# Optimization experiments

Hardware: AMD Instinct MI355X
Metric: run time of the kernel (lower is better)

The kernel has to match this reference:

```python
import jax, jax.numpy as jnp
import numpy as np

N_NODES = 100000
N_EDGES = 1600000
F_IN, F_HID, F_OUT = 128, 128, 16
NEG_SLOPE = 0.2


def _glorot(key, shape):
    fan = sum(shape)
    return jax.random.uniform(key, shape, jnp.float32, -1.0, 1.0) * jnp.sqrt(6.0 / fan)


def setup_inputs() -> dict:
    key = jax.random.key(0)
    ks = jax.random.split(key, 16)
    x = jax.random.normal(ks[0], (N_NODES, F_IN), jnp.float32)
    edge_index = jax.random.randint(ks[1], (2, N_EDGES), 0, N_NODES, jnp.int64)
    d1, d2, d3 = F_HID, F_HID // 2, F_OUT
    return {
        'x': x,
        'edge_index': edge_index,
        'W1': _glorot(ks[2], (F_IN, d1)), 'a_src1': _glorot(ks[3], (d1,)), 'a_dst1': _glorot(ks[4], (d1,)), 'b1': jnp.zeros((d1,), jnp.float32),
        'W2': _glorot(ks[5], (d1, d2)), 'a_src2': _glorot(ks[6], (d2,)), 'a_dst2': _glorot(ks[7], (d2,)), 'b2': jnp.zeros((d2,), jnp.float32),
        'W3': _glorot(ks[8], (d2, d3)), 'a_src3': _glorot(ks[9], (d3,)), 'a_dst3': _glorot(ks[10], (d3,)), 'b3': jnp.zeros((d3,), jnp.float32),
    }


def gat_conv(x, src, dst, W, a_s, a_d, b):
    # x: [N, Fin] -> h: [N, Fout]; src/dst: [E] (self-loops included)
    h = x @ W
    e = jax.nn.leaky_relu(h @ a_s, NEG_SLOPE * 0 + NEG_SLOPE)  # placeholder avoided below
    # attention logits per edge: leaky_relu(alpha_src[src] + alpha_dst[dst])
    al_s = h @ a_s  # [N]
    al_d = h @ a_d  # [N]
    logits = jax.nn.leaky_relu(al_s[src] + al_d[dst], NEG_SLOPE)  # [E]
    # numerically stable softmax over incoming edges of each dst node
    m = jax.ops.segment_max(logits, dst, num_segments=N_NODES)
    m = jnp.where(jnp.isfinite(m), m, 0.0)
    ex = jnp.exp(logits - m[dst])
    denom = jax.ops.segment_sum(ex, dst, num_segments=N_NODES)
    alpha = ex / denom[dst]  # self-loops guarantee denom > 0
    out = jax.ops.segment_sum(alpha[:, None] * h[src], dst, num_segments=N_NODES)
    return out + b


def reference(x, edge_index, W1, a_src1, a_dst1, b1, W2, a_src2, a_dst2, b2, W3, a_src3, a_dst3, b3):
    loops = jnp.arange(N_NODES, dtype=edge_index.dtype)
    src = jnp.concatenate([edge_index[0], loops])
    dst = jnp.concatenate([edge_index[1], loops])
    h = gat_conv(x, src, dst, W1, a_src1, a_dst1, b1)
    h = jax.nn.relu(h)  # dropout p=0.5 is identity in eval mode
    h = gat_conv(h, src, dst, W2, a_src2, a_dst2, b2)
    h = jax.nn.relu(h)
    out = gat_conv(h, src, dst, W3, a_src3, a_dst3, b3)
    return out
```

## Files before the change

### kernel.cpp

```cpp
#include <hip/hip_runtime.h>
#include <hip/hip_bf16.h>

typedef __hip_bfloat16 bf16;
typedef __attribute__((ext_vector_type(8))) __bf16 bf16x8;
typedef __attribute__((ext_vector_type(4))) float f32x4;

static constexpr int N = 100000;
static constexpr int E = 1600000;
static constexpr int ETOT = E + N;
static constexpr float SLOPE = 0.2f;

__device__ __constant__ int c_poff[12] = {0, 16384, 16512, 16640,
                                          16768, 24960, 25024, 25088,
                                          25152, 26176, 26192, 26208};
static constexpr int PTOT = 26224;
static constexpr int H_POFF[12] = {0, 16384, 16512, 16640, 16768, 24960,
                                   25024, 25088, 25152, 26176, 26192, 26208};

struct Src12 { const void* p[12]; };

__device__ __forceinline__ float bfLo(unsigned u) { return __uint_as_float(u << 16); }
__device__ __forceinline__ float bfHi(unsigned u) { return __uint_as_float(u & 0xFFFF0000u); }

__device__ __forceinline__ void fma8(const uint4 r, float e, float* acc) {
  acc[0] = fmaf(e, bfLo(r.x), acc[0]);
  acc[1] = fmaf(e, bfHi(r.x), acc[1]);
  acc[2] = fmaf(e, bfLo(r.y), acc[2]);
  acc[3] = fmaf(e, bfHi(r.y), acc[3]);
  acc[4] = fmaf(e, bfLo(r.z), acc[4]);
  acc[5] = fmaf(e, bfHi(r.z), acc[5]);
  acc[6] = fmaf(e, bfLo(r.w), acc[6]);
  acc[7] = fmaf(e, bfHi(r.w), acc[7]);
}

__device__ __forceinline__ float edge_ex(float l) {
  l = (l > 0.f) ? l : SLOPE * l;
  return __expf(l);
}

__device__ __forceinline__ void loadEdge(const int* __restrict__ ei32,
                                         const long long* __restrict__ ei64,
                                         int use64, int t, int& s, int& d) {
  if (t >= E) { s = d = t - E; return; }
  if (use64) { s = (int)ei64[t]; d = (int)ei64[E + t]; }
  else       { s = ei32[t];      d = ei32[E + t]; }
}

__device__ __forceinline__ unsigned pk2(float a, float b) {
  bf16 x = __float2bfloat16(a), y = __float2bfloat16(b);
  unsigned short ux = *(unsigned short*)&x, uy = *(unsigned short*)&y;
  return ((unsigned)uy << 16) | ux;
}

static constexpr int CHUNK = 8192;
static constexpr int NCHK  = (ETOT + CHUNK - 1) / CHUNK;
static constexpr int NB1   = (N + 511) / 512;
static constexpr int M1    = NB1 * NCHK;
static constexpr int SBLK  = (M1 + 255) / 256;

__global__ __launch_bounds__(256) void detect_kernel(
    const unsigned long long* __restrict__ ei64,
    const unsigned short* __restrict__ w1u16, int* __restrict__ flags) {
  const int t = threadIdx.x;
  __shared__ unsigned long long bl[4];
  __shared__ unsigned long long sb64;
  const int w = t >> 6;
  bool p64 = (t < 64) && (ei64[t] >= (unsigned long long)N);
  unsigned long long b64 = __ballot(p64);
  if (t == 0) sb64 = b64;
  bool pf = (((w1u16[t] >> 7) & 0xFFu) >= 126u);
  unsigned long long bf_ = __ballot(pf);
  if ((t & 63) == 0) bl[w] = bf_;
  __syncthreads();
  if (t == 0) {
    flags[0] = (sb64 == 0ull) ? 1 : 0;
    flags[1] = ((bl[0] | bl[1] | bl[2] | bl[3]) != 0ull) ? 1 : 0;
  }
}

static constexpr int PB_PAR = (PTOT + 255) / 256;
static constexpr int PB_W1  = 128 * 128 / 256;
static constexpr int PB_W2  = 128 * 64 / 256;
static constexpr int PB_W3  = 64 * 16 / 256;
static constexpr int PB_TOT = NCHK + PB_PAR + PB_W1 + PB_W2 + PB_W3;

__device__ __forceinline__ void conv_w(const void* W, int kd, int dout, int f32,
                                       bf16* __restrict__ wt, int idx) {
  int n = idx / kd, k = idx - n * kd;
  float v = f32 ? ((const float*)W)[k * dout + n]
                : __bfloat162float(((const bf16*)W)[k * dout + n]);
  wt[idx] = __float2bfloat16(v);
}

__global__ __launch_bounds__(256) void prep_kernel(
    const int* __restrict__ ei32, const long long* __restrict__ ei64,
    const int* __restrict__ flags, int* __restrict__ c1,
    Src12 s, float* __restrict__ prm,
    bf16* __restrict__ w1t, bf16* __restrict__ w2t, bf16* __restrict__ w3t) {
  const int b = blockIdx.x, tid = threadIdx.x;
  const int f64 = flags[0], f32 = flags[1];
  if (b < NCHK) {
    __shared__ int h1[NB1];
    if (tid < NB1) h1[tid] = 0;
    __syncthreads();
    const int t0 = b * CHUNK;
#pragma unroll 4
    for (int i = tid; i < CHUNK; i += 256) {
      int t = t0 + i;
      if (t < ETOT) {
        int d = (t >= E) ? (t - E) : (f64 ? (int)ei64[E + t] : ei32[E + t]);
        atomicAdd(&h1[d >> 9], 1);
      }
    }
    __syncthreads();
    if (tid < NB1) c1[tid * NCHK + b] = h1[tid];
  } else if (b < NCHK + PB_PAR) {
    int t = (b - NCHK) * 256 + tid;
    if (t < PTOT) {
      int k = 0;
#pragma unroll
      for (int i = 1; i < 12; ++i)
        if (t >= c_poff[i]) k = i;
      int j = t - c_poff[k];
      prm[t] = f32 ? ((const float*)s.p[k])[j]
                   : __bfloat162float(((const bf16*)s.p[k])[j]);
    }
  } else if (b < NCHK + PB_PAR + PB_W1) {
    conv_w(s.p[0], 128, 128, f32, w1t, (b - NCHK - PB_PAR) * 256 + tid);
  } else if (b < NCHK + PB_PAR + PB_W1 + PB_W2) {
    conv_w(s.p[4], 128, 64, f32, w2t, (b - NCHK - PB_PAR - PB_W1) * 256 + tid);
  } else {
    conv_w(s.p[8], 64, 16, f32, w3t, (b - NCHK - PB_PAR - PB_W1 - PB_W2) * 256 + tid);
  }
}

__global__ __launch_bounds__(256) void scanA_kernel(const int* __restrict__ c1,
                                                    int* __restrict__ bsum) {
  __shared__ int red[256];
  const int t = threadIdx.x;
  const int i = blockIdx.x * 256 + t;
  red[t] = (i < M1) ? c1[i] : 0;
  __syncthreads();
#pragma unroll
  for (int off = 128; off > 0; off >>= 1) {
    if (t < off) red[t] += red[t + off];
    __syncthreads();
  }
  if (t == 0) bsum[blockIdx.x] = red[0];
}

__global__ __launch_bounds__(256) void scanB_kernel(const int* __restrict__ bsum,
                                                    int* __restrict__ boff) {
  __shared__ int s[256];
  const int t = threadIdx.x;
  const int v = (t < SBLK) ? bsum[t] : 0;
  s[t] = v;
  __syncthreads();
  for (int off = 1; off < 256; off <<= 1) {
    int u = (t >= off) ? s[t - off] : 0;
    __syncthreads();
    s[t] += u;
    __syncthreads();
  }
  if (t < SBLK) boff[t] = s[t] - v;
}

__global__ __launch_bounds__(256) void scanC_kernel(const int* __restrict__ c1,
                                                    const int* __restrict__ boff,
                                                    int* __restrict__ off1) {
  __shared__ int s[256];
  const int t = threadIdx.x;
  const int i = blockIdx.x * 256 + t;
  const int v = (i < M1) ? c1[i] : 0;
  s[t] = v;
  __syncthreads();
#pragma unroll
  for (int off = 1; off < 256; off <<= 1) {
    int u = (t >= off) ? s[t - off] : 0;
    __syncthreads();
    s[t] += u;
    __syncthreads();
  }
  if (i < M1) off1[i] = boff[blockIdx.x] + s[t] - v;
}

__device__ __forceinline__ void phaseC_body(int c, const int* __restrict__ ei32,
                                            const long long* __restrict__ ei64,
                                            int f64, const int* __restrict__ off1,
                                            int2* __restrict__ tmp) {
  __shared__ int cur[NB1];
  const int tid = threadIdx.x;
  if (tid < NB1) cur[tid] = off1[tid * NCHK + c];
  __syncthreads();
  const int t0 = c * CHUNK;
#pragma unroll 4
  for (int i = tid; i < CHUNK; i += 256) {
    int t = t0 + i;
    if (t < ETOT) {
      int s, d;
      loadEdge(ei32, ei64, f64, t, s, d);
      int pos = atomicAdd(&cur[d >> 9], 1);
      tmp[pos] = make_int2(d, s);
    }
  }
}

__global__ __launch_bounds__(256) void phaseD_kernel(const int* __restrict__ off1,
                                                     const int2* __restrict__ tmp,
                                                     int* __restrict__ rowptr,
                                                     int* __restrict__ ssrt) {
  __shared__ int h2[512], e2[512], cur[512];
  __shared__ int ps[256];
  const int b = blockIdx.x, t = threadIdx.x;
  const int base = off1[b * NCHK];
  const int end = (b + 1 < NB1) ? off1[(b + 1) * NCHK] : ETOT;
  const int len = end - base;
  h2[2 * t] = 0; h2[2 * t + 1] = 0;
  __syncthreads();
  for (int i = t; i < len; i += 256)
    atomicAdd(&h2[tmp[base + i].x & 511], 1);
  __syncthreads();
  const int s1 = h2[2 * t], s2 = h2[2 * t + 1];
  ps[t] = s1 + s2;
  __syncthreads();
  for (int off = 1; off < 256; off <<= 1) {
    int u = (t >= off) ? ps[t - off] : 0;
    __syncthreads();
    ps[t] += u;
    __syncthreads();
  }
  const int ep = ps[t] - (s1 + s2);
  e2[2 * t] = ep;
  e2[2 * t + 1] = ep + s1;
  cur[2 * t] = ep;
  cur[2 * t + 1] = ep + s1;
  __syncthreads();
#pragma unroll
  for (int k = 0; k < 2; ++k) {
    int f = 2 * t + k;
    int node = (b << 9) + f;
    if (node < N) rowptr[node] = base + e2[f];
  }
  if (b == 0 && t == 0) rowptr[N] = ETOT;
  for (int i = t; i < len; i += 256) {
    int2 e = tmp[base + i];
    int pos = base + atomicAdd(&cur[e.x & 511], 1);
    ssrt[pos] = e.y;
  }
}

template <int KD, int DOUT, bool XD>
__device__ __forceinline__ void gemm_body(int bb, const void* __restrict__ inv,
                                          const int* __restrict__ flags,
                                          const unsigned short* __restrict__ wt,
                                          bf16* __restrict__ h,
                                          const float* __restrict__ a_s,
                                          const float* __restrict__ a_d,
                                          float* __restrict__ als,
                                          float* __restrict__ ald) {
  constexpr int SA = KD + 8;
  constexpr int NT = DOUT / 16;
  constexpr int KS = KD / 32;
  __shared__ unsigned short sA[64 * SA];
  __shared__ unsigned short sB[DOUT * SA];
  const int tid = threadIdx.x;
  const int m0 = bb * 64;
  for (int idx = tid; idx < DOUT * KD / 8; idx += 256) {
    int n = idx / (KD / 8), k8 = idx - n * (KD / 8);
    *(uint4*)(sB + n * SA + k8 * 8) = *(const uint4*)(wt + n * KD + k8 * 8);
  }
  const bool f32 = XD ? (flags[1] != 0) : false;
  for (int idx = tid; idx < 64 * KD / 8; idx += 256) {
    int r = idx / (KD / 8), k8 = idx - r * (KD / 8);
    int m = m0 + r;
    uint4 v = make_uint4(0, 0, 0, 0);
    if (m < N) {
      if (XD && f32) {
        const float4 v0 = *((const float4*)inv + ((size_t)m * KD + k8 * 8) / 4);
        const float4 v1 = *((const float4*)inv + ((size_t)m * KD + k8 * 8) / 4 + 1);
        v = make_uint4(pk2(v0.x, v0.y), pk2(v0.z, v0.w),
                       pk2(v1.x, v1.y), pk2(v1.z, v1.w));
      } else {
        v = *((const uint4*)inv + ((size_t)m * KD + k8 * 8) / 8);
      }
    }
    *(uint4*)(sA + r * SA + k8 * 8) = v;
  }
  __syncthreads();
  const int lane = tid & 63;
  const int wv = tid >> 6;
  const int lr = lane & 15;
  const int q = lane >> 4;
  f32x4 acc[NT];
#pragma unroll
  for (int t = 0; t < NT; ++t)
#pragma unroll
    for (int r = 0; r < 4; ++r) acc[t][r] = 0.f;
  const int arow = wv * 16 + lr;
#pragma unroll
  for (int ks = 0; ks < KS; ++ks) {
    const int k0 = ks * 32 + q * 8;
    const bf16x8 a = *(const bf16x8*)(sA + arow * SA + k0);
#pragma unroll
    for (int t = 0; t < NT; ++t) {
      const bf16x8 b = *(const bf16x8*)(sB + (t * 16 + lr) * SA + k0);
      acc[t] = __builtin_amdgcn_mfma_f32_16x16x32_bf16(a, b, acc[t], 0, 0, 0);
    }
  }
  float ps[4] = {0.f, 0.f, 0.f, 0.f}, pd[4] = {0.f, 0.f, 0.f, 0.f};
#pragma unroll
  for (int t = 0; t < NT; ++t) {
    const float av = a_s[t * 16 + lr];
    const float dv = a_d[t * 16 + lr];
#pragma unroll
    for (int r = 0; r < 4; ++r) {
      ps[r] = fmaf(acc[t][r], av, ps[r]);
      pd[r] = fmaf(acc[t][r], dv, pd[r]);
    }
  }
#pragma unroll
  for (int m = 1; m < 16; m <<= 1)
#pragma unroll
    for (int r = 0; r < 4; ++r) {
      ps[r] += __shfl_xor(ps[r], m, 64);
      pd[r] += __shfl_xor(pd[r], m, 64);
    }
  const int mb = m0 + wv * 16 + q * 4;
  if (lr == 0) {
#pragma unroll
    for (int r = 0; r < 4; ++r) {
      int m = mb + r;
      if (m < N) { als[m] = ps[r]; ald[m] = pd[r]; }
    }
  }
#pragma unroll
  for (int t = 0; t < NT; ++t)
#pragma unroll
    for (int r = 0; r < 4; ++r) {
      int m = mb + r;
      if (m < N) h[(size_t)m * DOUT + t * 16 + lr] = __float2bfloat16(acc[t][r]);
    }
}

template <int KD, int DOUT>
__global__ __launch_bounds__(256) void gemm_al(const unsigned short* __restrict__ inb,
                                               const unsigned short* __restrict__ wt,
                                               bf16* __restrict__ h,
                                               const float* __restrict__ a_s,
                                               const float* __restrict__ a_d,
                                               float* __restrict__ als,
                                               float* __restrict__ ald) {
  gemm_body<KD, DOUT, false>(blockIdx.x, inb, nullptr, wt, h, a_s, a_d, als, ald);
}

static constexpr int GB1 = (N + 63) / 64;

__global__ __launch_bounds__(256) void gemm1_phaseC(
    const void* __restrict__ x, const int* __restrict__ flags,
    const unsigned short* __restrict__ wt, bf16* __restrict__ h,
    const float* __restrict__ a_s, const float* __restrict__ a_d,
    float* __restrict__ als, float* __restrict__ ald,
    const int* __restrict__ ei32, const long long* __restrict__ ei64,
    const int* __restrict__ off1, int2* __restrict__ tmp) {
  if (blockIdx.x < GB1) {
    gemm_body<128, 128, true>(blockIdx.x, x, flags, wt, h, a_s, a_d, als, ald);
  } else {
    int c = blockIdx.x - GB1;
    if (c < NCHK) phaseC_body(c, ei32, ei64, flags[0], off1, tmp);
  }
}

template <int DOUT, bool RELU, bool FINAL>
__global__ __launch_bounds__(256) void aggregate_csr(const int* __restrict__ rowptr,
                                                     const int* __restrict__ ssrt,
                                                     const float* __restrict__ als,
                                                     const float* __restrict__ ald,
                                                     const unsigned short* __restrict__ hb,
                                                     const float* __restrict__ bias,
                                                     bf16* __restrict__ outb,
                                                     void* __restrict__ outv,
                                                     const int* __restrict__ flags) {
  constexpr int TPN = DOUT / 8;
  constexpr int NPB = 256 / TPN;
  const int sub = threadIdx.x % TPN;
  const int d = blockIdx.x * NPB + threadIdx.x / TPN;
  if (d >= N) return;
  const int p0 = rowptr[d], p1 = rowptr[d + 1];
  const float ad = ald[d];
  const int col0 = sub * 8;
  float acc[8];
#pragma unroll
  for (int c = 0; c < 8; ++c) acc[c] = 0.f;
  float sum = 0.f;
  int p = p0;
  for (; p + 4 <= p1; p += 4) {
    const int s0 = ssrt[p + 0];
    const int s1 = ssrt[p + 1];
    const int s2 = ssrt[p + 2];
    const int s3 = ssrt[p + 3];
    const uint4 r0 = *reinterpret_cast<const uint4*>(hb + (size_t)s0 * DOUT + col0);
    const uint4 r1 = *reinterpret_cast<const uint4*>(hb + (size_t)s1 * DOUT + col0);
    const uint4 r2 = *reinterpret_cast<const uint4*>(hb + (size_t)s2 * DOUT + col0);
    const uint4 r3 = *reinterpret_cast<const uint4*>(hb + (size_t)s3 * DOUT + col0);
    const float x0 = edge_ex(als[s0] + ad);
    const float x1 = edge_ex(als[s1] + ad);
    const float x2 = edge_ex(als[s2] + ad);
    const float x3 = edge_ex(als[s3] + ad);
    sum += (x0 + x1) + (x2 + x3);
    fma8(r0, x0, acc);
    fma8(r1, x1, acc);
    fma8(r2, x2, acc);
    fma8(r3, x3, acc);
  }
  for (; p < p1; ++p) {
    const int s = ssrt[p];
    const uint4 r = *reinterpret_cast<const uint4*>(hb + (size_t)s * DOUT + col0);
    const float x = edge_ex(als[s] + ad);
    sum += x;
    fma8(r, x, acc);
  }
  const float inv = 1.f / sum;
  if (FINAL) {
    const bool f32o = flags[1] != 0;
#pragma unroll
    for (int c = 0; c < 8; ++c) {
      float v = acc[c] * inv + bias[col0 + c];
      if (f32o) ((float*)outv)[(size_t)d * DOUT + col0 + c] = v;
      else      ((bf16*)outv)[(size_t)d * DOUT + col0 + c] = __float2bfloat16(v);
    }
  } else {
#pragma unroll
    for (int c = 0; c < 8; ++c) {
      float v = acc[c] * inv + bias[col0 + c];
      if (RELU) v = (v > 0.f) ? v : 0.f;
      outb[(size_t)d * DOUT + col0 + c] = __float2bfloat16(v);
    }
  }
}

static inline size_t rup(size_t v) { return (v + 255) & ~(size_t)255; }

extern "C" void kernel_launch(void* const* d_in, const int* in_sizes, int n_in,
                              void* d_out, int out_size, void* d_ws, size_t ws_size,
                              hipStream_t stream) {
  const int* ei32 = (const int*)d_in[1];
  const long long* ei64 = (const long long*)d_in[1];

  char* p = (char*)d_ws;
  int*   flags  = (int*)p;   p += 256;
  float* prm    = (float*)p; p += rup((size_t)PTOT * 4);
  bf16*  w1t    = (bf16*)p;  p += rup((size_t)128 * 128 * 2);
  bf16*  w2t    = (bf16*)p;  p += rup((size_t)128 * 64 * 2);
  bf16*  w3t    = (bf16*)p;  p += rup((size_t)64 * 16 * 2);
  float* als    = (float*)p; p += rup((size_t)N * 4);
  float* ald    = (float*)p; p += rup((size_t)N * 4);
  int*   rowptr = (int*)p;   p += rup((size_t)(N + 1) * 4);
  int*   c1     = (int*)p;   p += rup((size_t)M1 * 4);
  int*   off1   = (int*)p;   p += rup((size_t)M1 * 4);
  int*   bsum   = (int*)p;   p += rup((size_t)SBLK * 4);
  int*   boff   = (int*)p;   p += rup((size_t)SBLK * 4);
  int2*  tmp    = (int2*)p;  p += rup((size_t)ETOT * 8);
  int*   ssrt   = (int*)p;   p += rup((size_t)ETOT * 4);
  bf16*  obuf   = (bf16*)p;  p += rup((size_t)N * 128 * 2);
  bf16*  hbuf   = (bf16*)p;

  Src12 s;
  for (int i = 0; i < 12; ++i) s.p[i] = d_in[2 + i];

  detect_kernel<<<1, 256, 0, stream>>>(
      (const unsigned long long*)d_in[1], (const unsigned short*)d_in[2], flags);
  prep_kernel<<<PB_TOT, 256, 0, stream>>>(ei32, ei64, flags, c1, s, prm, w1t, w2t, w3t);
  scanA_kernel<<<SBLK, 256, 0, stream>>>(c1, bsum);
  scanB_kernel<<<1, 256, 0, stream>>>(bsum, boff);
  scanC_kernel<<<SBLK, 256, 0, stream>>>(c1, boff, off1);

  const float *as1 = prm + H_POFF[1], *ad1 = prm + H_POFF[2], *b1 = prm + H_POFF[3];
  const float *as2 = prm + H_POFF[5], *ad2 = prm + H_POFF[6], *b2 = prm + H_POFF[7];
  const float *as3 = prm + H_POFF[9], *ad3 = prm + H_POFF[10], *b3 = prm + H_POFF[11];

  gemm1_phaseC<<<GB1 + NCHK, 256, 0, stream>>>(
      d_in[0], flags, (const unsigned short*)w1t, hbuf, as1, ad1, als, ald,
      ei32, ei64, off1, tmp);
  phaseD_kernel<<<NB1, 256, 0, stream>>>(off1, tmp, rowptr, ssrt);
  aggregate_csr<128, true, false><<<(N + 15) / 16, 256, 0, stream>>>(
      rowptr, ssrt, als, ald, (const unsigned short*)hbuf, b1, obuf, nullptr, flags);
  gemm_al<128, 64><<<GB1, 256, 0, stream>>>(
      (const unsigned short*)obuf, (const unsigned short*)w2t, hbuf, as2, ad2, als, ald);
  aggregate_csr<64, true, false><<<(N + 31) / 32, 256, 0, stream>>>(
      rowptr, ssrt, als, ald, (const unsigned short*)hbuf, b2, obuf, nullptr, flags);
  gemm_al<64, 16><<<GB1, 256, 0, stream>>>(
      (const unsigned short*)obuf, (const unsigned short*)w3t, hbuf, as3, ad3, als, ald);
  aggregate_csr<16, false, true><<<(N + 127) / 128, 256, 0, stream>>>(
      rowptr, ssrt, als, ald, (const unsigned short*)hbuf, b3, nullptr, d_out, flags);
}
```

Baseline: 336.8 us.

## Fuse post-scan GAT stages into one cooperative persistent kernel with grid syncs

Replaces the separate gemm1/phaseC, phaseD, three aggregate and two GEMM launches with a single cooperative persistent kernel. The stages are separated by grid.sync and each stage walks its work units in a grid-stride loop, with shared memory carved from one static buffer. The intent is to remove launch gaps and per-kernel tail effects. The layer-1 GEMM now reads B fragments straight from global memory instead of staging the weights in LDS. The costs are a grid size capped by occupancy, the overhead of each grid barrier, possibly lower occupancy from the larger combined register and LDS footprint, and uncached global B loads in the first GEMM.

```diff
diff --git a/kernel.cpp b/kernel.cpp
--- a/kernel.cpp
+++ b/kernel.cpp
@@ -1,5 +1,8 @@
 #include <hip/hip_runtime.h>
 #include <hip/hip_bf16.h>
+#include <hip/hip_cooperative_groups.h>
+
+namespace cg = cooperative_groups;
 
 typedef __hip_bfloat16 bf16;
 typedef __attribute__((ext_vector_type(8))) __bf16 bf16x8;
@@ -187,8 +190,8 @@
 __device__ __forceinline__ void phaseC_body(int c, const int* __restrict__ ei32,
                                             const long long* __restrict__ ei64,
                                             int f64, const int* __restrict__ off1,
-                                            int2* __restrict__ tmp) {
-  __shared__ int cur[NB1];
+                                            int2* __restrict__ tmp, int* sm) {
+  int* cur = sm;
   const int tid = threadIdx.x;
   if (tid < NB1) cur[tid] = off1[tid * NCHK + c];
   __syncthreads();
@@ -205,13 +208,15 @@
   }
 }
 
-__global__ __launch_bounds__(256) void phaseD_kernel(const int* __restrict__ off1,
-                                                     const int2* __restrict__ tmp,
-                                                     int* __restrict__ rowptr,
-                                                     int* __restrict__ ssrt) {
-  __shared__ int h2[512], e2[512], cur[512];
-  __shared__ int ps[256];
-  const int b = blockIdx.x, t = threadIdx.x;
+__device__ __forceinline__ void phaseD_body(int b, const int* __restrict__ off1,
+                                            const int2* __restrict__ tmp,
+                                            int* __restrict__ rowptr,
+                                            int* __restrict__ ssrt, int* sm) {
+  int* h2 = sm;
+  int* e2 = sm + 512;
+  int* cur = sm + 1024;
+  int* ps = sm + 1536;
+  const int t = threadIdx.x;
   const int base = off1[b * NCHK];
   const int end = (b + 1 < NB1) ? off1[(b + 1) * NCHK] : ETOT;
   const int len = end - base;
@@ -249,7 +254,7 @@
   }
 }
 
-template <int KD, int DOUT, bool XD>
+template <int KD, int DOUT, bool XD, bool BG>
 __device__ __forceinline__ void gemm_body(int bb, const void* __restrict__ inv,
                                           const int* __restrict__ flags,
                                           const unsigned short* __restrict__ wt,
@@ -257,17 +262,18 @@
                                           const float* __restrict__ a_s,
                                           const float* __restrict__ a_d,
                                           float* __restrict__ als,
-                                          float* __restrict__ ald) {
+                                          float* __restrict__ ald,
+                                          unsigned short* sA, unsigned short* sB) {
   constexpr int SA = KD + 8;
   constexpr int NT = DOUT / 16;
   constexpr int KS = KD / 32;
-  __shared__ unsigned short sA[64 * SA];
-  __shared__ unsigned short sB[DOUT * SA];
   const int tid = threadIdx.x;
   const int m0 = bb * 64;
-  for (int idx = tid; idx < DOUT * KD / 8; idx += 256) {
-    int n = idx / (KD / 8), k8 = idx - n * (KD / 8);
-    *(uint4*)(sB + n * SA + k8 * 8) = *(const uint4*)(wt + n * KD + k8 * 8);
+  if (!BG) {
+    for (int idx = tid; idx < DOUT * KD / 8; idx += 256) {
+      int n = idx / (KD / 8), k8 = idx - n * (KD / 8);
+      *(uint4*)(sB + n * SA + k8 * 8) = *(const uint4*)(wt + n * KD + k8 * 8);
+    }
   }
   const bool f32 = XD ? (flags[1] != 0) : false;
   for (int idx = tid; idx < 64 * KD / 8; idx += 256) {
@@ -303,7 +309,8 @@
     const bf16x8 a = *(const bf16x8*)(sA + arow * SA + k0);
 #pragma unroll
     for (int t = 0; t < NT; ++t) {
-      const bf16x8 b = *(const bf16x8*)(sB + (t * 16 + lr) * SA + k0);
+      const bf16x8 b = BG ? *(const bf16x8*)(wt + (t * 16 + lr) * KD + k0)
+                          : *(const bf16x8*)(sB + (t * 16 + lr) * SA + k0);
       acc[t] = __builtin_amdgcn_mfma_f32_16x16x32_bf16(a, b, acc[t], 0, 0, 0);
     }
   }
@@ -342,48 +349,20 @@
     }
 }
 
-template <int KD, int DOUT>
-__global__ __launch_bounds__(256) void gemm_al(const unsigned short* __restrict__ inb,
-                                               const unsigned short* __restrict__ wt,
-                                               bf16* __restrict__ h,
-                                               const float* __restrict__ a_s,
-                                               const float* __restrict__ a_d,
-                                               float* __restrict__ als,
-                                               float* __restrict__ ald) {
-  gemm_body<KD, DOUT, false>(blockIdx.x, inb, nullptr, wt, h, a_s, a_d, als, ald);
-}
-
-static constexpr int GB1 = (N + 63) / 64;
-
-__global__ __launch_bounds__(256) void gemm1_phaseC(
-    const void* __restrict__ x, const int* __restrict__ flags,
-    const unsigned short* __restrict__ wt, bf16* __restrict__ h,
-    const float* __restrict__ a_s, const float* __restrict__ a_d,
-    float* __restrict__ als, float* __restrict__ ald,
-    const int* __restrict__ ei32, const long long* __restrict__ ei64,
-    const int* __restrict__ off1, int2* __restrict__ tmp) {
-  if (blockIdx.x < GB1) {
-    gemm_body<128, 128, true>(blockIdx.x, x, flags, wt, h, a_s, a_d, als, ald);
-  } else {
-    int c = blockIdx.x - GB1;
-    if (c < NCHK) phaseC_body(c, ei32, ei64, flags[0], off1, tmp);
-  }
-}
-
 template <int DOUT, bool RELU, bool FINAL>
-__global__ __launch_bounds__(256) void aggregate_csr(const int* __restrict__ rowptr,
-                                                     const int* __restrict__ ssrt,
-                                                     const float* __restrict__ als,
-                                                     const float* __restrict__ ald,
-                                                     const unsigned short* __restrict__ hb,
-                                                     const float* __restrict__ bias,
-                                                     bf16* __restrict__ outb,
-                                                     void* __restrict__ outv,
-                                                     const int* __restrict__ flags) {
+__device__ __forceinline__ void agg_body(int bb, const int* __restrict__ rowptr,
+                                         const int* __restrict__ ssrt,
+                                         const float* __restrict__ als,
+                                         const float* __restrict__ ald,
+                                         const unsigned short* __restrict__ hb,
+                                         const float* __restrict__ bias,
+                                         bf16* __restrict__ outb,
+                                         void* __restrict__ outv,
+                                         const int* __restrict__ flags) {
   constexpr int TPN = DOUT / 8;
   constexpr int NPB = 256 / TPN;
   const int sub = threadIdx.x % TPN;
-  const int d = blockIdx.x * NPB + threadIdx.x / TPN;
+  const int d = bb * NPB + threadIdx.x / TPN;
   if (d >= N) return;
   const int p0 = rowptr[d], p1 = rowptr[d + 1];
   const float ad = ald[d];
@@ -438,6 +417,69 @@
   }
 }
 
+static constexpr int GB1 = (N + 63) / 64;
+static constexpr int AG1 = (N + 15) / 16;
+static constexpr int AG2 = (N + 31) / 32;
+static constexpr int AG3 = (N + 127) / 128;
+
+struct MArgs {
+  const int* ei32; const long long* ei64; const int* flags;
+  const int* off1; int2* tmp; int* rowptr; int* ssrt;
+  const void* x;
+  const unsigned short* w1t; const unsigned short* w2t; const unsigned short* w3t;
+  const float *as1, *ad1, *b1, *as2, *ad2, *b2, *as3, *ad3, *b3;
+  bf16* hbuf; bf16* obuf; float* als; float* ald; void* dout;
+};
+
+__global__ __launch_bounds__(256, 4) void mega_kernel(MArgs a) {
+  cg::grid_group grid = cg::this_grid();
+  __shared__ __align__(16) char smem[34816];
+  unsigned short* sA = (unsigned short*)smem;
+  unsigned short* sB = (unsigned short*)(smem + 17408);
+  const int nb = gridDim.x;
+
+  for (int u = blockIdx.x; u < GB1 + NCHK; u += nb) {
+    if (u < GB1)
+      gemm_body<128, 128, true, true>(u, a.x, a.flags, a.w1t, a.hbuf,
+                                      a.as1, a.ad1, a.als, a.ald, sA, sB);
+    else
+      phaseC_body(u - GB1, a.ei32, a.ei64, a.flags[0], a.off1, a.tmp, (int*)smem);
+    __syncthreads();
+  }
+  grid.sync();
+  for (int u = blockIdx.x; u < NB1; u += nb) {
+    phaseD_body(u, a.off1, a.tmp, a.rowptr, a.ssrt, (int*)smem);
+    __syncthreads();
+  }
+  grid.sync();
+  for (int u = blockIdx.x; u < AG1; u += nb)
+    agg_body<128, true, false>(u, a.rowptr, a.ssrt, a.als, a.ald,
+                               (const unsigned short*)a.hbuf, a.b1, a.obuf,
+                               nullptr, a.flags);
+  grid.sync();
+  for (int u = blockIdx.x; u < GB1; u += nb) {
+    gemm_body<128, 64, false, false>(u, a.obuf, a.flags, a.w2t, a.hbuf,
+                                     a.as2, a.ad2, a.als, a.ald, sA, sB);
+    __syncthreads();
+  }
+  grid.sync();
+  for (int u = blockIdx.x; u < AG2; u += nb)
+    agg_body<64, true, false>(u, a.rowptr, a.ssrt, a.als, a.ald,
+                              (const unsigned short*)a.hbuf, a.b2, a.obuf,
+                              nullptr, a.flags);
+  grid.sync();
+  for (int u = blockIdx.x; u < GB1; u += nb) {
+    gemm_body<64, 16, false, false>(u, a.obuf, a.flags, a.w3t, a.hbuf,
+                                    a.as3, a.ad3, a.als, a.ald, sA, sB);
+    __syncthreads();
+  }
+  grid.sync();
+  for (int u = blockIdx.x; u < AG3; u += nb)
+    agg_body<16, false, true>(u, a.rowptr, a.ssrt, a.als, a.ald,
+                              (const unsigned short*)a.hbuf, a.b3, nullptr,
+                              a.dout, a.flags);
+}
+
 static inline size_t rup(size_t v) { return (v + 255) & ~(size_t)255; }
 
 extern "C" void kernel_launch(void* const* d_in, const int* in_sizes, int n_in,
@@ -474,22 +516,31 @@
   scanB_kernel<<<1, 256, 0, stream>>>(bsum, boff);
   scanC_kernel<<<SBLK, 256, 0, stream>>>(c1, boff, off1);
 
-  const float *as1 = prm + H_POFF[1], *ad1 = prm + H_POFF[2], *b1 = prm + H_POFF[3];
-  const float *as2 = prm + H_POFF[5], *ad2 = prm + H_POFF[6], *b2 = prm + H_POFF[7];
-  const float *as3 = prm + H_POFF[9], *ad3 = prm + H_POFF[10], *b3 = prm + H_POFF[11];
-
-  gemm1_phaseC<<<GB1 + NCHK, 256, 0, stream>>>(
-      d_in[0], flags, (const unsigned short*)w1t, hbuf, as1, ad1, als, ald,
-      ei32, ei64, off1, tmp);
-  phaseD_kernel<<<NB1, 256, 0, stream>>>(off1, tmp, rowptr, ssrt);
-  aggregate_csr<128, true, false><<<(N + 15) / 16, 256, 0, stream>>>(
-      rowptr, ssrt, als, ald, (const unsigned short*)hbuf, b1, obuf, nullptr, flags);
-  gemm_al<128, 64><<<GB1, 256, 0, stream>>>(
-      (const unsigned short*)obuf, (const unsigned short*)w2t, hbuf, as2, ad2, als, ald);
-  aggregate_csr<64, true, false><<<(N + 31) / 32, 256, 0, stream>>>(
-      rowptr, ssrt, als, ald, (const unsigned short*)hbuf, b2, obuf, nullptr, flags);
-  gemm_al<64, 16><<<GB1, 256, 0, stream>>>(
-      (const unsigned short*)obuf, (const unsigned short*)w3t, hbuf, as3, ad3, als, ald);
-  aggregate_csr<16, false, true><<<(N + 127) / 128, 256, 0, stream>>>(
-      rowptr, ssrt, als, ald, (const unsigned short*)hbuf, b3, nullptr, d_out, flags);
-}
+  MArgs ma;
+  ma.ei32 = ei32; ma.ei64 = ei64; ma.flags = flags;
+  ma.off1 = off1; ma.tmp = tmp; ma.rowptr = rowptr; ma.ssrt = ssrt;
+  ma.x = d_in[0];
+  ma.w1t = (const unsigned short*)w1t;
+  ma.w2t = (const unsigned short*)w2t;
+  ma.w3t = (const unsigned short*)w3t;
+  ma.as1 = prm + H_POFF[1];  ma.ad1 = prm + H_POFF[2];  ma.b1 = prm + H_POFF[3];
+  ma.as2 = prm + H_POFF[5];  ma.ad2 = prm + H_POFF[6];  ma.b2 = prm + H_POFF[7];
+  ma.as3 = prm + H_POFF[9];  ma.ad3 = prm + H_POFF[10]; ma.b3 = prm + H_POFF[11];
+  ma.hbuf = hbuf; ma.obuf = obuf; ma.als = als; ma.ald = ald; ma.dout = d_out;
+
+  int nblk = 0;
+  hipError_t e1 = hipOccupancyMaxActiveBlocksPerMultiprocessor(
+      &nblk, (const void*)mega_kernel, 256, 0);
+  if (e1 != hipSuccess || nblk < 1) nblk = 2;
+  int ncu = 256;
+  int dev = 0;
+  if (hipGetDevice(&dev) == hipSuccess) {
+    hipError_t e2 = hipDeviceGetAttribute(&ncu, hipDeviceAttributeMultiprocessorCount, dev);
+    if (e2 != hipSuccess || ncu < 1) ncu = 256;
+  }
+  int grid = nblk * ncu;
+  void* kargs[] = {&ma};
+  hipError_t e3 = hipLaunchCooperativeKernel((void*)mega_kernel, dim3(grid),
+                                             dim3(256), kargs, 0, stream);
+  (void)e3;
+}
```

Result: slower. 815.7 us (+142.2%).

## Fuse layer aggregation with next layer's GEMM and attention projections

Applied to the files above, without the earlier changes.

Each layer's CSR softmax aggregation now writes its ReLU'd bf16 rows into shared memory, and the same block runs the next layer's MFMA GEMM plus the attention-score dot products on them. This removes the global round trip of the intermediate activation buffer and two kernel launches. Separate per-layer buffers are used so a layer never reads h or alpha arrays that the same kernel is writing. The cost is 512-thread blocks with larger shared-memory use and a gather phase whose latency can no longer overlap with other blocks' GEMM work as freely.

```diff
diff --git a/kernel.cpp b/kernel.cpp
--- a/kernel.cpp
+++ b/kernel.cpp
@@ -342,17 +342,6 @@
     }
 }
 
-template <int KD, int DOUT>
-__global__ __launch_bounds__(256) void gemm_al(const unsigned short* __restrict__ inb,
-                                               const unsigned short* __restrict__ wt,
-                                               bf16* __restrict__ h,
-                                               const float* __restrict__ a_s,
-                                               const float* __restrict__ a_d,
-                                               float* __restrict__ als,
-                                               float* __restrict__ ald) {
-  gemm_body<KD, DOUT, false>(blockIdx.x, inb, nullptr, wt, h, a_s, a_d, als, ald);
-}
-
 static constexpr int GB1 = (N + 63) / 64;
 
 __global__ __launch_bounds__(256) void gemm1_phaseC(
@@ -370,16 +359,148 @@
   }
 }
 
-template <int DOUT, bool RELU, bool FINAL>
-__global__ __launch_bounds__(256) void aggregate_csr(const int* __restrict__ rowptr,
-                                                     const int* __restrict__ ssrt,
-                                                     const float* __restrict__ als,
-                                                     const float* __restrict__ ald,
-                                                     const unsigned short* __restrict__ hb,
-                                                     const float* __restrict__ bias,
-                                                     bf16* __restrict__ outb,
-                                                     void* __restrict__ outv,
-                                                     const int* __restrict__ flags) {
+static constexpr int AB = (N + 127) / 128;
+
+template <int DA, int DOUT>
+__global__ __launch_bounds__(512) void aggemm_kernel(
+    const int* __restrict__ rowptr, const int* __restrict__ ssrt,
+    const float* __restrict__ als_in, const float* __restrict__ ald_in,
+    const unsigned short* __restrict__ hin, const float* __restrict__ bias,
+    const unsigned short* __restrict__ wt, bf16* __restrict__ hout,
+    const float* __restrict__ a_s, const float* __restrict__ a_d,
+    float* __restrict__ als_out, float* __restrict__ ald_out) {
+  constexpr int SA = DA + 8;
+  constexpr int TPN = DA / 8;
+  constexpr int NPR = 512 / TPN;
+  constexpr int NR = 128 / NPR;
+  constexpr int NT = DOUT / 16;
+  constexpr int KS = DA / 32;
+  __shared__ unsigned short sA[128 * SA];
+  __shared__ unsigned short sB[DOUT * SA];
+  const int tid = threadIdx.x;
+  const int m0 = blockIdx.x * 128;
+  for (int idx = tid; idx < DOUT * DA / 8; idx += 512) {
+    int n = idx / (DA / 8), k8 = idx - n * (DA / 8);
+    *(uint4*)(sB + n * SA + k8 * 8) = *(const uint4*)(wt + n * DA + k8 * 8);
+  }
+  const int sub = tid % TPN;
+  const int rr0 = tid / TPN;
+  const int col0 = sub * 8;
+#pragma unroll
+  for (int r = 0; r < NR; ++r) {
+    const int row = r * NPR + rr0;
+    const int d = m0 + row;
+    if (d < N) {
+      const int p0 = rowptr[d], p1 = rowptr[d + 1];
+      const float ad = ald_in[d];
+      float acc[8];
+#pragma unroll
+      for (int c = 0; c < 8; ++c) acc[c] = 0.f;
+      float sum = 0.f;
+      int p = p0;
+      for (; p + 4 <= p1; p += 4) {
+        const int s0 = ssrt[p + 0];
+        const int s1 = ssrt[p + 1];
+        const int s2 = ssrt[p + 2];
+        const int s3 = ssrt[p + 3];
+        const uint4 r0 = *reinterpret_cast<const uint4*>(hin + (size_t)s0 * DA + col0);
+        const uint4 r1 = *reinterpret_cast<const uint4*>(hin + (size_t)s1 * DA + col0);
+        const uint4 r2 = *reinterpret_cast<const uint4*>(hin + (size_t)s2 * DA + col0);
+        const uint4 r3 = *reinterpret_cast<const uint4*>(hin + (size_t)s3 * DA + col0);
+        const float x0 = edge_ex(als_in[s0] + ad);
+        const float x1 = edge_ex(als_in[s1] + ad);
+        const float x2 = edge_ex(als_in[s2] + ad);
+        const float x3 = edge_ex(als_in[s3] + ad);
+        sum += (x0 + x1) + (x2 + x3);
+        fma8(r0, x0, acc);
+        fma8(r1, x1, acc);
+        fma8(r2, x2, acc);
+        fma8(r3, x3, acc);
+      }
+      for (; p < p1; ++p) {
+        const int s = ssrt[p];
+        const uint4 rr = *reinterpret_cast<const uint4*>(hin + (size_t)s * DA + col0);
+        const float x = edge_ex(als_in[s] + ad);
+        sum += x;
+        fma8(rr, x, acc);
+      }
+      const float inv = 1.f / sum;
+      float v[8];
+#pragma unroll
+      for (int c = 0; c < 8; ++c) {
+        float w = acc[c] * inv + bias[col0 + c];
+        v[c] = (w > 0.f) ? w : 0.f;
+      }
+      uint4 pk = make_uint4(pk2(v[0], v[1]), pk2(v[2], v[3]),
+                            pk2(v[4], v[5]), pk2(v[6], v[7]));
+      *(uint4*)(sA + row * SA + col0) = pk;
+    }
+  }
+  __syncthreads();
+  const int lane = tid & 63;
+  const int wv = tid >> 6;
+  const int lr = lane & 15;
+  const int q = lane >> 4;
+  f32x4 acc[NT];
+#pragma unroll
+  for (int t = 0; t < NT; ++t)
+#pragma unroll
+    for (int r = 0; r < 4; ++r) acc[t][r] = 0.f;
+  const int arow = wv * 16 + lr;
+#pragma unroll
+  for (int ks = 0; ks < KS; ++ks) {
+    const int k0 = ks * 32 + q * 8;
+    const bf16x8 a = *(const bf16x8*)(sA + arow * SA + k0);
+#pragma unroll
+    for (int t = 0; t < NT; ++t) {
+      const bf16x8 b = *(const bf16x8*)(sB + (t * 16 + lr) * SA + k0);
+      acc[t] = __builtin_amdgcn_mfma_f32_16x16x32_bf16(a, b, acc[t], 0, 0, 0);
+    }
+  }
+  float ps[4] = {0.f, 0.f, 0.f, 0.f}, pd[4] = {0.f, 0.f, 0.f, 0.f};
+#pragma unroll
+  for (int t = 0; t < NT; ++t) {
+    const float av = a_s[t * 16 + lr];
+    const float dv = a_d[t * 16 + lr];
+#pragma unroll
+    for (int r = 0; r < 4; ++r) {
+      ps[r] = fmaf(acc[t][r], av, ps[r]);
+      pd[r] = fmaf(acc[t][r], dv, pd[r]);
+    }
+  }
+#pragma unroll
+  for (int m = 1; m < 16; m <<= 1)
+#pragma unroll
+    for (int r = 0; r < 4; ++r) {
+      ps[r] += __shfl_xor(ps[r], m, 64);
+      pd[r] += __shfl_xor(pd[r], m, 64);
+    }
+  const int mb = m0 + wv * 16 + q * 4;
+  if (lr == 0) {
+#pragma unroll
+    for (int r = 0; r < 4; ++r) {
+      int m = mb + r;
+      if (m < N) { als_out[m] = ps[r]; ald_out[m] = pd[r]; }
+    }
+  }
+#pragma unroll
+  for (int t = 0; t < NT; ++t)
+#pragma unroll
+    for (int r = 0; r < 4; ++r) {
+      int m = mb + r;
+      if (m < N) hout[(size_t)m * DOUT + t * 16 + lr] = __float2bfloat16(acc[t][r]);
+    }
+}
+
+template <int DOUT>
+__global__ __launch_bounds__(256) void agg_final(const int* __restrict__ rowptr,
+                                                 const int* __restrict__ ssrt,
+                                                 const float* __restrict__ als,
+                                                 const float* __restrict__ ald,
+                                                 const unsigned short* __restrict__ hb,
+                                                 const float* __restrict__ bias,
+                                                 void* __restrict__ outv,
+                                                 const int* __restrict__ flags) {
   constexpr int TPN = DOUT / 8;
   constexpr int NPB = 256 / TPN;
   const int sub = threadIdx.x % TPN;
@@ -420,21 +541,12 @@
     fma8(r, x, acc);
   }
   const float inv = 1.f / sum;
-  if (FINAL) {
-    const bool f32o = flags[1] != 0;
-#pragma unroll
-    for (int c = 0; c < 8; ++c) {
-      float v = acc[c] * inv + bias[col0 + c];
-      if (f32o) ((float*)outv)[(size_t)d * DOUT + col0 + c] = v;
-      else      ((bf16*)outv)[(size_t)d * DOUT + col0 + c] = __float2bfloat16(v);
-    }
-  } else {
-#pragma unroll
-    for (int c = 0; c < 8; ++c) {
-      float v = acc[c] * inv + bias[col0 + c];
-      if (RELU) v = (v > 0.f) ? v : 0.f;
-      outb[(size_t)d * DOUT + col0 + c] = __float2bfloat16(v);
-    }
+  const bool f32o = flags[1] != 0;
+#pragma unroll
+  for (int c = 0; c < 8; ++c) {
+    float v = acc[c] * inv + bias[col0 + c];
+    if (f32o) ((float*)outv)[(size_t)d * DOUT + col0 + c] = v;
+    else      ((bf16*)outv)[(size_t)d * DOUT + col0 + c] = __float2bfloat16(v);
   }
 }
 
@@ -452,8 +564,12 @@
   bf16*  w1t    = (bf16*)p;  p += rup((size_t)128 * 128 * 2);
   bf16*  w2t    = (bf16*)p;  p += rup((size_t)128 * 64 * 2);
   bf16*  w3t    = (bf16*)p;  p += rup((size_t)64 * 16 * 2);
-  float* als    = (float*)p; p += rup((size_t)N * 4);
-  float* ald    = (float*)p; p += rup((size_t)N * 4);
+  float* als1   = (float*)p; p += rup((size_t)N * 4);
+  float* ald1   = (float*)p; p += rup((size_t)N * 4);
+  float* als2   = (float*)p; p += rup((size_t)N * 4);
+  float* ald2   = (float*)p; p += rup((size_t)N * 4);
+  float* als3   = (float*)p; p += rup((size_t)N * 4);
+  float* ald3   = (float*)p; p += rup((size_t)N * 4);
   int*   rowptr = (int*)p;   p += rup((size_t)(N + 1) * 4);
   int*   c1     = (int*)p;   p += rup((size_t)M1 * 4);
   int*   off1   = (int*)p;   p += rup((size_t)M1 * 4);
@@ -461,8 +577,9 @@
   int*   boff   = (int*)p;   p += rup((size_t)SBLK * 4);
   int2*  tmp    = (int2*)p;  p += rup((size_t)ETOT * 8);
   int*   ssrt   = (int*)p;   p += rup((size_t)ETOT * 4);
-  bf16*  obuf   = (bf16*)p;  p += rup((size_t)N * 128 * 2);
-  bf16*  hbuf   = (bf16*)p;
+  bf16*  h1     = (bf16*)p;  p += rup((size_t)N * 128 * 2);
+  bf16*  h2     = (bf16*)p;  p += rup((size_t)N * 64 * 2);
+  bf16*  h3     = (bf16*)p;
 
   Src12 s;
   for (int i = 0; i < 12; ++i) s.p[i] = d_in[2 + i];
@@ -479,17 +596,15 @@
   const float *as3 = prm + H_POFF[9], *ad3 = prm + H_POFF[10], *b3 = prm + H_POFF[11];
 
   gemm1_phaseC<<<GB1 + NCHK, 256, 0, stream>>>(
-      d_in[0], flags, (const unsigned short*)w1t, hbuf, as1, ad1, als, ald,
+      d_in[0], flags, (const unsigned short*)w1t, h1, as1, ad1, als1, ald1,
       ei32, ei64, off1, tmp);
   phaseD_kernel<<<NB1, 256, 0, stream>>>(off1, tmp, rowptr, ssrt);
-  aggregate_csr<128, true, false><<<(N + 15) / 16, 256, 0, stream>>>(
-      rowptr, ssrt, als, ald, (const unsigned short*)hbuf, b1, obuf, nullptr, flags);
-  gemm_al<128, 64><<<GB1, 256, 0, stream>>>(
-      (const unsigned short*)obuf, (const unsigned short*)w2t, hbuf, as2, ad2, als, ald);
-  aggregate_csr<64, true, false><<<(N + 31) / 32, 256, 0, stream>>>(
-      rowptr, ssrt, als, ald, (const unsigned short*)hbuf, b2, obuf, nullptr, flags);
-  gemm_al<64, 16><<<GB1, 256, 0, stream>>>(
-      (const unsigned short*)obuf, (const unsigned short*)w3t, hbuf, as3, ad3, als, ald);
-  aggregate_csr<16, false, true><<<(N + 127) / 128, 256, 0, stream>>>(
-      rowptr, ssrt, als, ald, (const unsigned short*)hbuf, b3, nullptr, d_out, flags);
-}
+  aggemm_kernel<128, 64><<<AB, 512, 0, stream>>>(
+      rowptr, ssrt, als1, ald1, (const unsigned short*)h1, b1,
+      (const unsigned short*)w2t, h2, as2, ad2, als2, ald2);
+  aggemm_kernel<64, 16><<<AB, 512, 0, stream>>>(
+      rowptr, ssrt, als2, ald2, (const unsigned short*)h2, b2,
+      (const unsigned short*)w3t, h3, as3, ad3, als3, ald3);
+  agg_final<16><<<(N + 127) / 128, 256, 0, stream>>>(
+      rowptr, ssrt, als3, ald3, (const unsigned short*)h3, b3, d_out, flags);
+}
```

Measured after the change: 343.9 us. 2.1% more time.
